# Performance work log

Hardware: AMD Instinct MI355X
Metric: run time of the kernel (lower is better)

The kernel has to match this reference:

```python
import jax, jax.numpy as jnp
import numpy as np

MEM_DIM = 2048
MEM_FEAT = 512
N_TOKENS = 65536
ALPHA = 0.1
SOFTMAX_SCALE = 10.0


def _l2_normalize(x, axis, eps=1e-12):
    # matches tf.math.l2_normalize: x / sqrt(max(sum(x^2), eps))
    sq = jnp.sum(jnp.square(x), axis=axis, keepdims=True)
    return x * jax.lax.rsqrt(jnp.maximum(sq, eps))


def setup_inputs() -> dict:
    key = jax.random.key(0)
    k1, k2 = jax.random.split(key)
    inputs = jax.random.normal(k1, (N_TOKENS, MEM_FEAT), dtype=jnp.float32)
    memory = jax.random.normal(k2, (MEM_DIM, MEM_FEAT), dtype=jnp.float32) * 0.05
    return {"inputs": inputs, "memory": memory}


def reference(inputs, memory):
    inputs_norm = _l2_normalize(inputs, axis=1)            # [N, F]
    memory_norm = _l2_normalize(memory, axis=1)            # [M, F]
    cos_sim = jnp.einsum('nf,mf->nm', inputs_norm, memory_norm)  # [N, M]
    attn = jax.nn.softmax(cos_sim * SOFTMAX_SCALE, axis=1)       # [N, M]
    mem_update = jnp.einsum('nm,mf->nf', attn, memory_norm)      # [N, F]
    closest_idx = jnp.argmax(attn, axis=1)                       # [N]
    # one_hot^T @ inputs_norm == segment-sum of inputs_norm by closest code
    memory_updates = jax.ops.segment_sum(inputs_norm, closest_idx,
                                         num_segments=MEM_DIM)  # [M, F]
    updated_memory = memory * (1.0 - ALPHA) + memory_updates * ALPHA
    return mem_update, updated_memory
```

## Files before the change

### kernel.cpp

```cpp
#include <hip/hip_runtime.h>
#include <stdint.h>

#define N_TOK   65536
#define MDIM    2048
#define FDIM    512
#define SCALE_F 10.0f
#define TAU_BF  1.2e-3f
#define TAU_SP  2e-5f
#define QCAP    8192

typedef __attribute__((ext_vector_type(8))) unsigned short u16x8;
typedef __attribute__((ext_vector_type(4))) unsigned short u16x4;
typedef __attribute__((ext_vector_type(8))) __bf16 bf16x8;
typedef __attribute__((ext_vector_type(4))) float f32x4;

__device__ __forceinline__ unsigned short f2bf(float f) {
  unsigned int u = __builtin_bit_cast(unsigned int, f);
  u += 0x7fffu + ((u >> 16) & 1u);
  return (unsigned short)(u >> 16);
}
__device__ __forceinline__ float bf2f(unsigned short b) {
  return __builtin_bit_cast(float, (unsigned int)b << 16);
}
__device__ __forceinline__ f32x4 mfma16(u16x8 a, u16x8 b, f32x4 c) {
  return __builtin_amdgcn_mfma_f32_16x16x32_bf16(
      __builtin_bit_cast(bf16x8, a), __builtin_bit_cast(bf16x8, b), c, 0, 0, 0);
}
__device__ __forceinline__ void gload16(const unsigned short* g, unsigned short* l) {
  __builtin_amdgcn_global_load_lds(
      (const __attribute__((address_space(1))) unsigned int*)g,
      (__attribute__((address_space(3))) unsigned int*)l,
      16, 0, 0);
}
__device__ __forceinline__ unsigned long long packkey(float x, int col) {
  unsigned u = __builtin_bit_cast(unsigned, x);
  u = (u & 0x80000000u) ? ~u : (u | 0x80000000u);
  return ((unsigned long long)u << 32) | (unsigned)(2048 - col);
}
__device__ __forceinline__ float unpackval(unsigned long long k) {
  unsigned u = (unsigned)(k >> 32);
  u = (u & 0x80000000u) ? (u & 0x7fffffffu) : ~u;
  return __builtin_bit_cast(float, u);
}
__device__ __forceinline__ int unpackcol(unsigned long long k) {
  return 2048 - (int)(k & 0xffffffffu);
}
__device__ __forceinline__ void merge2(unsigned long long& k1, unsigned long long& k2,
                                       unsigned long long o1, unsigned long long o2) {
  if (o1 > k1) { k2 = (k1 > o2) ? k1 : o2; k1 = o1; }
  else if (o1 > k2) { k2 = o1; }
}

__global__ __launch_bounds__(64) void zero_k(int* __restrict__ qcount) {
  if (threadIdx.x == 0) *qcount = 0;
}

__global__ __launch_bounds__(64) void prep_memory_k(
    const float* __restrict__ mem, unsigned short* __restrict__ Bh,
    unsigned short* __restrict__ Bl) {
  const int m = blockIdx.x;
  const int lane = threadIdx.x;
  const float* row = mem + (size_t)m * FDIM;
  float4 a = *(const float4*)(row + lane * 4);
  float4 b = *(const float4*)(row + 256 + lane * 4);
  float s = a.x * a.x + a.y * a.y + a.z * a.z + a.w * a.w +
            b.x * b.x + b.y * b.y + b.z * b.z + b.w * b.w;
  #pragma unroll
  for (int off = 1; off < 64; off <<= 1) s += __shfl_xor(s, off);
  const float rn = 1.0f / sqrtf(fmaxf(s, 1e-12f));
  float v[8] = {a.x, a.y, a.z, a.w, b.x, b.y, b.z, b.w};
  #pragma unroll
  for (int h = 0; h < 2; ++h) {
    ushort4 hs, lo;
    #pragma unroll
    for (int q = 0; q < 4; ++q) {
      float x = v[h * 4 + q] * rn;
      unsigned short hb = f2bf(x);
      ((unsigned short*)&hs)[q] = hb;
      ((unsigned short*)&lo)[q] = f2bf(x - bf2f(hb));
    }
    const size_t e = (size_t)m * FDIM + h * 256 + lane * 4;
    *(ushort4*)(Bh + e) = hs;
    *(ushort4*)(Bl + e) = lo;
  }
}

__global__ __launch_bounds__(256) void transpose_k(
    const unsigned short* __restrict__ Bh, unsigned short* __restrict__ Bt) {
  __shared__ unsigned short t[32][33];
  const int m0 = blockIdx.x * 32, f0 = blockIdx.y * 32;
  const int tx = threadIdx.x & 31, ty = threadIdx.x >> 5;
  #pragma unroll
  for (int r = ty; r < 32; r += 8)
    t[r][tx] = Bh[(size_t)(m0 + r) * FDIM + f0 + tx];
  __syncthreads();
  #pragma unroll
  for (int r = ty; r < 32; r += 8)
    Bt[(size_t)(f0 + r) * MDIM + m0 + tx] = t[tx][r];
}

__global__ __launch_bounds__(256) void prep_a_k(
    const float* __restrict__ inp, float* __restrict__ inv_n,
    unsigned short* __restrict__ Ah, int baseRow) {
  const int r = blockIdx.x * 4 + (threadIdx.x >> 6);
  const int lane = threadIdx.x & 63;
  const int grow = baseRow + r;
  const float* x = inp + (size_t)grow * FDIM;
  float4 a = *(const float4*)(x + lane * 4);
  float4 b = *(const float4*)(x + 256 + lane * 4);
  float s = a.x * a.x + a.y * a.y + a.z * a.z + a.w * a.w +
            b.x * b.x + b.y * b.y + b.z * b.z + b.w * b.w;
  #pragma unroll
  for (int off = 1; off < 64; off <<= 1) s += __shfl_xor(s, off);
  const float rn = 1.0f / sqrtf(fmaxf(s, 1e-12f));
  if (lane == 0) inv_n[grow] = rn;
  ushort4 h0, h1;
  h0.x = f2bf(a.x * rn); h0.y = f2bf(a.y * rn);
  h0.z = f2bf(a.z * rn); h0.w = f2bf(a.w * rn);
  h1.x = f2bf(b.x * rn); h1.y = f2bf(b.y * rn);
  h1.z = f2bf(b.z * rn); h1.w = f2bf(b.w * rn);
  *(ushort4*)(Ah + (size_t)r * FDIM + lane * 4) = h0;
  *(ushort4*)(Ah + (size_t)r * FDIM + 256 + lane * 4) = h1;
}

template <int MODE>
__global__ __launch_bounds__(512) void gemm8p_k(
    const unsigned short* __restrict__ Am, const unsigned short* __restrict__ Bm,
    void* __restrict__ Cv, int N, int K, int nbxLog2,
    float* __restrict__ ssum, unsigned long long* __restrict__ sk1,
    unsigned long long* __restrict__ sk2, const float* __restrict__ rowinv) {
  __shared__ alignas(16) char smem[131072];
  int wg = blockIdx.x;
  { const int q = gridDim.x >> 3; wg = (wg & 7) * q + (wg >> 3); }
  const int bx = wg & ((1 << nbxLog2) - 1);
  const int by = wg >> nbxLog2;
  const int m0 = by * 256, n0 = bx * 256;
  const int tid = threadIdx.x;
  const int lane = tid & 63, wid = tid >> 6;
  const int wm = wid >> 2, wn = wid & 3;
  const int lr = lane & 15, ls = lane >> 4;
  const int c16 = (lane & 7) ^ (lane >> 3);
  const int lrow8 = lane >> 3;

  f32x4 acc[8][4] = {};
  u16x8 bF[4][2];

  const int NT = K >> 6;
  const int niter = NT >> 1;

  auto stageB = [&](int t, int half) {
    char* dst0 = smem + (t & 1) * 65536 + 32768 + half * 16384;
    #pragma unroll
    for (int c = 0; c < 2; ++c) {
      const int R = (wid * 2 + c) * 8;
      const int rg = n0 + half * 128 + R + lrow8;
      gload16(Bm + (size_t)rg * K + t * 64 + c16 * 8,
              (unsigned short*)(dst0 + R * 128));
    }
  };
  auto stageA = [&](int t, int q) {
    const int half = wid >> 2;
    const int R = q * 32 + (wid & 3) * 8;
    char* dst = smem + (t & 1) * 65536 + half * 16384 + R * 128;
    const int rg = m0 + half * 128 + R + lrow8;
    gload16(Am + (size_t)rg * K + t * 64 + c16 * 8, (unsigned short*)dst);
  };
  auto ldsA = [&](int b, int rl, int ks) -> u16x8 {
    const int p = (ks * 4 + ls) ^ (rl & 7);
    return *(const u16x8*)(smem + b * 65536 + wm * 16384 + rl * 128 + p * 16);
  };
  auto ldsB = [&](int b, int rlb, int ks) -> u16x8 {
    const int half = rlb >> 7, rl = rlb & 127;
    const int p = (ks * 4 + ls) ^ (rl & 7);
    return *(const u16x8*)(smem + b * 65536 + 32768 + half * 16384 + rl * 128 + p * 16);
  };

  stageB(0, 0); stageB(0, 1);
  stageA(0, 0); stageA(0, 1); stageA(0, 2); stageA(0, 3);
  stageB(1, 0); stageB(1, 1);
  stageA(1, 0); stageA(1, 1); stageA(1, 2);

  for (int it = 0; it < niter; ++it) {
    const int T0 = 2 * it, T1 = T0 + 1;
    #pragma unroll
    for (int ph = 0; ph < 8; ++ph) {
      const int tb = (ph < 4) ? 0 : 1;
      const int ql = ph & 3;
      if (ql == 0) {
        if (ph == 4 && it == niter - 1)
          asm volatile("s_waitcnt vmcnt(0)" ::: "memory");
        else
          asm volatile("s_waitcnt vmcnt(7)" ::: "memory");
        __builtin_amdgcn_sched_barrier(0);
        __builtin_amdgcn_s_barrier();
        #pragma unroll
        for (int nj = 0; nj < 4; ++nj)
          #pragma unroll
          for (int ks = 0; ks < 2; ++ks)
            bF[nj][ks] = ldsB(tb, wn * 64 + nj * 16 + lr, ks);
      } else {
        __builtin_amdgcn_s_barrier();
      }
      u16x8 aF[2][2];
      #pragma unroll
      for (int di = 0; di < 2; ++di)
        #pragma unroll
        for (int ks = 0; ks < 2; ++ks)
          aF[di][ks] = ldsA(tb, ql * 32 + di * 16 + lr, ks);
      if (ph == 0) { if (T1 < NT) stageA(T1, 3); }
      if (ph == 1) { if (T0 + 2 < NT) stageB(T0 + 2, 0); }
      if (ph == 2) { if (T0 + 2 < NT) { stageB(T0 + 2, 1); stageA(T0 + 2, 0); } }
      if (ph == 3) { if (T0 + 2 < NT) { stageA(T0 + 2, 1); stageA(T0 + 2, 2); } }
      if (ph == 4) { if (T0 + 2 < NT) stageA(T0 + 2, 3); }
      if (ph == 5) { if (T1 + 2 < NT) stageB(T1 + 2, 0); }
      if (ph == 6) { if (T1 + 2 < NT) { stageB(T1 + 2, 1); stageA(T1 + 2, 0); } }
      if (ph == 7) { if (T1 + 2 < NT) { stageA(T1 + 2, 1); stageA(T1 + 2, 2); } }
      __builtin_amdgcn_s_setprio(1);
      #pragma unroll
      for (int di = 0; di < 2; ++di)
        #pragma unroll
        for (int nj = 0; nj < 4; ++nj)
          #pragma unroll
          for (int ks = 0; ks < 2; ++ks)
            acc[ql * 2 + di][nj] = mfma16(aF[di][ks], bF[nj][ks], acc[ql * 2 + di][nj]);
      __builtin_amdgcn_s_setprio(0);
      __builtin_amdgcn_s_barrier();
    }
  }

  if constexpr (MODE == 1) {
    asm volatile("s_waitcnt vmcnt(0)" ::: "memory");
    __builtin_amdgcn_sched_barrier(0);
    __builtin_amdgcn_s_barrier();
    unsigned short* P = (unsigned short*)Cv;
    float* sc = (float*)smem;
    #pragma unroll
    for (int g = 0; g < 8; ++g) {
      if ((wid >> 2) == (g >> 2)) {
        const int di0 = (g & 3) * 2;
        #pragma unroll
        for (int di = 0; di < 2; ++di)
          #pragma unroll
          for (int nj = 0; nj < 4; ++nj)
            #pragma unroll
            for (int q = 0; q < 4; ++q)
              sc[(di * 16 + ls * 4 + q) * 260 + wn * 64 + nj * 16 + lr] =
                  acc[di0 + di][nj][q];
      }
      __syncthreads();
      {
        const int r = tid >> 4, cs = tid & 15;
        const int grow = m0 + g * 32 + r;
        float esum = 0.f, m1v = -3.4e38f, m2v = -3.4e38f;
        int c1 = 0;
        unsigned short pk[16];
        #pragma unroll
        for (int k = 0; k < 4; ++k) {
          const f32x4 v = *(const f32x4*)&sc[r * 260 + cs * 16 + k * 4];
          #pragma unroll
          for (int e = 0; e < 4; ++e) {
            const float s = v[e];
            const int col = n0 + cs * 16 + k * 4 + e;
            if (s > m1v) { m2v = m1v; m1v = s; c1 = col; }
            else if (s > m2v) m2v = s;
            const float ex = __expf(SCALE_F * s);
            esum += ex;
            pk[k * 4 + e] = f2bf(ex);
          }
        }
        *(u16x8*)&P[(size_t)grow * N + n0 + cs * 16] = *(u16x8*)&pk[0];
        *(u16x8*)&P[(size_t)grow * N + n0 + cs * 16 + 8] = *(u16x8*)&pk[8];
        unsigned long long k1 = packkey(m1v, c1);
        unsigned long long k2 = packkey(m2v, 2047);
        #pragma unroll
        for (int off = 1; off < 16; off <<= 1) {
          const unsigned long long o1 = __shfl_xor(k1, off);
          const unsigned long long o2 = __shfl_xor(k2, off);
          esum += __shfl_xor(esum, off);
          merge2(k1, k2, o1, o2);
        }
        if (cs == 0) {
          const size_t sp = (size_t)grow * 8 + bx;
          ssum[sp] = esum; sk1[sp] = k1; sk2[sp] = k2;
        }
      }
      __syncthreads();
    }
  } else {
    float* C = (float*)Cv;
    #pragma unroll
    for (int mi = 0; mi < 8; ++mi) {
      const int rbase = m0 + wm * 128 + mi * 16 + ls * 4;
      #pragma unroll
      for (int q = 0; q < 4; ++q) {
        const float ri = rowinv[rbase + q];
        #pragma unroll
        for (int nj = 0; nj < 4; ++nj) {
          const int col = n0 + wn * 64 + nj * 16 + lr;
          C[(size_t)(rbase + q) * N + col] = acc[mi][nj][q] * ri;
        }
      }
    }
  }
}

__global__ __launch_bounds__(256) void gemm_ref_k(
    const unsigned short* __restrict__ Ah, const unsigned short* __restrict__ Al,
    const unsigned short* __restrict__ Bh, const unsigned short* __restrict__ Bl,
    float* __restrict__ C, int N, int K, int nbxLog2,
    const int* __restrict__ qlimit) {
  const int wg = blockIdx.x;
  const int bx = wg & ((1 << nbxLog2) - 1);
  const int by = wg >> nbxLog2;
  const int m0 = by * 128, n0 = bx * 128;
  {
    int lim = *qlimit; if (lim > QCAP) lim = QCAP;
    lim = (lim + 127) & ~127;
    if (m0 >= lim) return;
  }
  constexpr int BUF_B = 4 * 8192;
  __shared__ alignas(16) char smem[2 * BUF_B];

  const int tid = threadIdx.x;
  const int lane = tid & 63, wave = tid >> 6;
  const int wr = wave >> 1, wc = wave & 1;
  const int lr = lane & 15, ls = lane >> 4;

  f32x4 acc[4][4] = {};

  const int row0 = wave * 32 + (lane >> 2);
  const int row1 = row0 + 16;
  const int ce = (lane & 3) * 8;
  const unsigned short* gA0 = Ah + (size_t)(m0 + row0) * K + ce;
  const unsigned short* gA1 = Ah + (size_t)(m0 + row1) * K + ce;
  const unsigned short* gB0 = Bh + (size_t)(n0 + row0) * K + ce;
  const unsigned short* gB1 = Bh + (size_t)(n0 + row1) * K + ce;
  const unsigned short* gAl0 = Al + (size_t)(m0 + row0) * K + ce;
  const unsigned short* gAl1 = Al + (size_t)(m0 + row1) * K + ce;
  const unsigned short* gBl0 = Bl + (size_t)(n0 + row0) * K + ce;
  const unsigned short* gBl1 = Bl + (size_t)(n0 + row1) * K + ce;

  auto stage = [&](int buf) {
    char* sb = smem + buf * BUF_B;
    unsigned short* bAh = (unsigned short*)sb;
    unsigned short* bBh = (unsigned short*)(sb + 8192);
    unsigned short* bAl = (unsigned short*)(sb + 16384);
    unsigned short* bBl = (unsigned short*)(sb + 24576);
    gload16(gA0, &bAh[wave * 1024]); gload16(gA1, &bAh[wave * 1024 + 512]);
    gload16(gB0, &bBh[wave * 1024]); gload16(gB1, &bBh[wave * 1024 + 512]);
    gload16(gAl0, &bAl[wave * 1024]); gload16(gAl1, &bAl[wave * 1024 + 512]);
    gload16(gBl0, &bBl[wave * 1024]); gload16(gBl1, &bBl[wave * 1024 + 512]);
    gA0 += 32; gA1 += 32; gB0 += 32; gB1 += 32;
    gAl0 += 32; gAl1 += 32; gBl0 += 32; gBl1 += 32;
  };

  const int nk = K >> 5;
  stage(0);
  __syncthreads();
  for (int ks = 0; ks < nk; ++ks) {
    const int cur = ks & 1;
    if (ks + 1 < nk) stage(cur ^ 1);
    const char* sb = smem + cur * BUF_B;
    u16x8 fa[4], fb[4], fal[4], fbl[4];
    #pragma unroll
    for (int i = 0; i < 4; ++i) {
      const int ra = (wr * 64 + i * 16 + lr) * 32 + ls * 8;
      const int rb = (wc * 64 + i * 16 + lr) * 32 + ls * 8;
      fa[i] = *(const u16x8*)&((const unsigned short*)sb)[ra];
      fb[i] = *(const u16x8*)&((const unsigned short*)(sb + 8192))[rb];
      fal[i] = *(const u16x8*)&((const unsigned short*)(sb + 16384))[ra];
      fbl[i] = *(const u16x8*)&((const unsigned short*)(sb + 24576))[rb];
    }
    #pragma unroll
    for (int i = 0; i < 4; ++i)
      #pragma unroll
      for (int j = 0; j < 4; ++j) {
        acc[i][j] = mfma16(fa[i], fb[j], acc[i][j]);
        acc[i][j] = mfma16(fal[i], fb[j], acc[i][j]);
        acc[i][j] = mfma16(fa[i], fbl[j], acc[i][j]);
      }
    __syncthreads();
  }

  #pragma unroll
  for (int i = 0; i < 4; ++i) {
    const int rrow = m0 + wr * 64 + i * 16 + ls * 4;
    #pragma unroll
    for (int j = 0; j < 4; ++j) {
      const int col = n0 + wc * 64 + j * 16 + lr;
      #pragma unroll
      for (int q = 0; q < 4; ++q)
        C[(size_t)(rrow + q) * N + col] = acc[i][j][q];
    }
  }
}

__global__ __launch_bounds__(256) void rowstat_k(
    const float* __restrict__ ssum, const unsigned long long* __restrict__ sk1,
    const unsigned long long* __restrict__ sk2, int* __restrict__ idx,
    float* __restrict__ rowinv, int* __restrict__ queue,
    int* __restrict__ qcount, int baseRow) {
  const int row = blockIdx.x * 32 + (threadIdx.x >> 3);
  const int p = threadIdx.x & 7;
  const size_t sp = (size_t)row * 8 + p;
  float sum = ssum[sp];
  unsigned long long k1 = sk1[sp], k2 = sk2[sp];
  #pragma unroll
  for (int off = 1; off < 8; off <<= 1) {
    const unsigned long long o1 = __shfl_xor(k1, off);
    const unsigned long long o2 = __shfl_xor(k2, off);
    sum += __shfl_xor(sum, off);
    merge2(k1, k2, o1, o2);
  }
  if (p == 0) {
    const int tok = baseRow + row;
    idx[tok] = unpackcol(k1);
    rowinv[row] = 1.0f / sum;
    if (unpackval(k1) - unpackval(k2) < TAU_BF) {
      int slot = atomicAdd(qcount, 1);
      if (slot < QCAP) queue[slot] = tok;
    }
  }
}

__global__ __launch_bounds__(256) void gather_prep_k(
    const int* __restrict__ queue, const int* __restrict__ qcount,
    const float* __restrict__ inp, const float* __restrict__ inv_n,
    unsigned short* __restrict__ Qh, unsigned short* __restrict__ Ql) {
  const int w = blockIdx.x * 4 + (threadIdx.x >> 6);
  const int lane = threadIdx.x & 63;
  int cnt = *qcount; if (cnt > QCAP) cnt = QCAP;
  if (w >= cnt) return;
  const int tok = queue[w];
  const float rn = inv_n[tok];
  const float* x = inp + (size_t)tok * FDIM;
  #pragma unroll
  for (int h = 0; h < 2; ++h) {
    float4 xv = *(const float4*)(x + h * 256 + lane * 4);
    float vv[4] = {xv.x, xv.y, xv.z, xv.w};
    ushort4 hs, lo;
    #pragma unroll
    for (int q = 0; q < 4; ++q) {
      float v = vv[q] * rn;
      unsigned short hb = f2bf(v);
      ((unsigned short*)&hs)[q] = hb;
      ((unsigned short*)&lo)[q] = f2bf(v - bf2f(hb));
    }
    const size_t e = (size_t)w * FDIM + h * 256 + lane * 4;
    *(ushort4*)(Qh + e) = hs;
    *(ushort4*)(Ql + e) = lo;
  }
}

__global__ __launch_bounds__(256) void refine2_k(
    const int* __restrict__ queue, const int* __restrict__ qcount,
    const float* __restrict__ Sref, const float* __restrict__ inp,
    const float* __restrict__ mem, int* __restrict__ idx) {
  const int w = blockIdx.x * 4 + (threadIdx.x >> 6);
  const int lane = threadIdx.x & 63;
  int cnt = *qcount; if (cnt > QCAP) cnt = QCAP;
  if (w >= cnt) return;
  const int tok = queue[w];
  const float* srow = Sref + (size_t)w * MDIM;
  float m1 = -3.4e38f, m2 = -3.4e38f;
  int i1 = 0x7fffffff, i2 = 0x7fffffff;
  #pragma unroll
  for (int i = 0; i < 8; ++i) {
    const float4 vv = *(const float4*)(srow + i * 256 + lane * 4);
    const float xs[4] = {vv.x, vv.y, vv.z, vv.w};
    #pragma unroll
    for (int q = 0; q < 4; ++q) {
      const float x = xs[q];
      const int ii = i * 256 + lane * 4 + q;
      if (x > m1 || (x == m1 && ii < i1)) { m2 = m1; i2 = i1; m1 = x; i1 = ii; }
      else if (x > m2 || (x == m2 && ii < i2)) { m2 = x; i2 = ii; }
    }
  }
  #pragma unroll
  for (int off = 1; off < 64; off <<= 1) {
    const float n1 = __shfl_xor(m1, off), n2 = __shfl_xor(m2, off);
    const int j1 = __shfl_xor(i1, off), j2 = __shfl_xor(i2, off);
    if (n1 > m1 || (n1 == m1 && j1 < i1)) {
      if (m1 > n2 || (m1 == n2 && i1 < j2)) { m2 = m1; i2 = i1; }
      else { m2 = n2; i2 = j2; }
      m1 = n1; i1 = j1;
    } else if (n1 > m2 || (n1 == m2 && j1 < i2)) { m2 = n1; i2 = j1; }
  }
  int pick = i1;
  if (m1 - m2 < TAU_SP) {
    const int a = (i1 < i2) ? i1 : i2, b = (i1 < i2) ? i2 : i1;
    const float* x = inp + (size_t)tok * FDIM;
    const float* ma = mem + (size_t)a * FDIM;
    const float* mb = mem + (size_t)b * FDIM;
    double da = 0, db = 0, na = 0, nb = 0;
    #pragma unroll
    for (int j = 0; j < 8; ++j) {
      const int e = lane * 8 + j;
      const double xv = x[e], av = ma[e], bv = mb[e];
      da += xv * av; na += av * av;
      db += xv * bv; nb += bv * bv;
    }
    #pragma unroll
    for (int off = 1; off < 64; off <<= 1) {
      da += __shfl_xor(da, off); na += __shfl_xor(na, off);
      db += __shfl_xor(db, off); nb += __shfl_xor(nb, off);
    }
    const double d1 = da / sqrt(fmax(na, 1e-12));
    const double d2 = db / sqrt(fmax(nb, 1e-12));
    if (d2 > d1) pick = b;
    else pick = a;
  }
  if (lane == 0) idx[tok] = pick;
}

__global__ __launch_bounds__(256) void segsum_k(
    const int* __restrict__ idx, const float* __restrict__ inp,
    const float* __restrict__ inv_n, float* __restrict__ updates) {
  __shared__ int lst[256];
  __shared__ int lcnt;
  const int m = blockIdx.x;
  const int t = threadIdx.x;
  float a0 = 0.f, a1 = 0.f;
  for (int base = 0; base < N_TOK; base += 4096) {
    if (t == 0) lcnt = 0;
    __syncthreads();
    #pragma unroll
    for (int u = 0; u < 4; ++u) {
      const int off4 = (u * 256 + t) * 4;
      const int4 v = *(const int4*)&idx[base + off4];
      if (v.x == m) { int p = atomicAdd(&lcnt, 1); if (p < 256) lst[p] = base + off4 + 0; }
      if (v.y == m) { int p = atomicAdd(&lcnt, 1); if (p < 256) lst[p] = base + off4 + 1; }
      if (v.z == m) { int p = atomicAdd(&lcnt, 1); if (p < 256) lst[p] = base + off4 + 2; }
      if (v.w == m) { int p = atomicAdd(&lcnt, 1); if (p < 256) lst[p] = base + off4 + 3; }
    }
    __syncthreads();
    int c = lcnt; if (c > 256) c = 256;
    if (t == 0 && c > 1) {
      for (int i = 1; i < c; ++i) {
        int key = lst[i], j = i - 1;
        while (j >= 0 && lst[j] > key) { lst[j + 1] = lst[j]; --j; }
        lst[j + 1] = key;
      }
    }
    __syncthreads();
    for (int i = 0; i < c; ++i) {
      const int tok = lst[i];
      const float rn = inv_n[tok];
      const float2 xv = *(const float2*)&inp[(size_t)tok * FDIM + t * 2];
      a0 += xv.x * rn; a1 += xv.y * rn;
    }
    __syncthreads();
  }
  *(float2*)&updates[(size_t)m * FDIM + t * 2] = make_float2(a0, a1);
}

__global__ __launch_bounds__(256) void final_update_k(
    const float* __restrict__ mem, const float* __restrict__ upd,
    float* __restrict__ out) {
  const size_t i = ((size_t)blockIdx.x * 256 + threadIdx.x) * 4;
  float4 m = *(const float4*)(mem + i);
  float4 u = *(const float4*)(upd + i);
  float4 r;
  r.x = m.x * 0.9f + u.x * 0.1f;
  r.y = m.y * 0.9f + u.y * 0.1f;
  r.z = m.z * 0.9f + u.z * 0.1f;
  r.w = m.w * 0.9f + u.w * 0.1f;
  *(float4*)(out + i) = r;
}

extern "C" void kernel_launch(void* const* d_in, const int* in_sizes, int n_in,
                              void* d_out, int out_size, void* d_ws, size_t ws_size,
                              hipStream_t stream) {
  const float* inputs = (const float*)d_in[0];
  const float* memory = (const float*)d_in[1];
  if (n_in >= 2 && in_sizes[0] != N_TOK * FDIM) {
    inputs = (const float*)d_in[1];
    memory = (const float*)d_in[0];
  }
  float* out_mu = (float*)d_out;
  float* out_um = out_mu + (size_t)N_TOK * FDIM;

  char* base = (char*)d_ws;
  size_t off = 0;
  auto take = [&](size_t bytes) -> char* {
    char* p = base + off;
    off = (off + bytes + 255) & ~(size_t)255;
    return p;
  };
  unsigned short* Bh = (unsigned short*)take((size_t)MDIM * FDIM * 2);
  unsigned short* Bl = (unsigned short*)take((size_t)MDIM * FDIM * 2);
  unsigned short* Bt = (unsigned short*)take((size_t)MDIM * FDIM * 2);
  float* inv_n = (float*)take((size_t)N_TOK * 4);
  float* updates = (float*)take((size_t)MDIM * FDIM * 4);
  int* idx = (int*)take((size_t)N_TOK * 4);
  int* queue = (int*)take((size_t)QCAP * 4);
  int* qcount = (int*)take(256);
  unsigned short* Qh = (unsigned short*)take((size_t)QCAP * FDIM * 2);
  unsigned short* Ql = (unsigned short*)take((size_t)QCAP * FDIM * 2);
  float* Sref = (float*)take((size_t)QCAP * MDIM * 4);
  const size_t fixed = off;

  int chunkT = 65536;
  while (chunkT > 2048 && fixed + (size_t)chunkT * 5400 + 8192 > ws_size)
    chunkT >>= 1;
  if (fixed + (size_t)chunkT * 5400 + 8192 > ws_size) return;

  unsigned short* Ah = (unsigned short*)take((size_t)chunkT * FDIM * 2);
  unsigned short* Pbuf = (unsigned short*)take((size_t)chunkT * MDIM * 2);
  float* ssum = (float*)take((size_t)chunkT * 8 * 4);
  unsigned long long* sk1 = (unsigned long long*)take((size_t)chunkT * 8 * 8);
  unsigned long long* sk2 = (unsigned long long*)take((size_t)chunkT * 8 * 8);
  float* rowinv = (float*)take((size_t)chunkT * 4);

  zero_k<<<1, 64, 0, stream>>>(qcount);
  prep_memory_k<<<MDIM, 64, 0, stream>>>(memory, Bh, Bl);
  transpose_k<<<dim3(MDIM / 32, FDIM / 32), 256, 0, stream>>>(Bh, Bt);

  for (int baseRow = 0; baseRow < N_TOK; baseRow += chunkT) {
    prep_a_k<<<chunkT / 4, 256, 0, stream>>>(inputs, inv_n, Ah, baseRow);
    gemm8p_k<1><<<(chunkT / 256) * 8, 512, 0, stream>>>(
        Ah, Bh, (void*)Pbuf, MDIM, FDIM, 3, ssum, sk1, sk2, nullptr);
    rowstat_k<<<chunkT / 32, 256, 0, stream>>>(
        ssum, sk1, sk2, idx, rowinv, queue, qcount, baseRow);
    gemm8p_k<2><<<(chunkT / 256) * 2, 512, 0, stream>>>(
        Pbuf, Bt, (void*)(out_mu + (size_t)baseRow * FDIM), FDIM, MDIM, 1,
        nullptr, nullptr, nullptr, rowinv);
  }
  gather_prep_k<<<QCAP / 4, 256, 0, stream>>>(queue, qcount, inputs, inv_n, Qh, Ql);
  gemm_ref_k<<<16 * (QCAP / 128), 256, 0, stream>>>(
      Qh, Ql, Bh, Bl, Sref, MDIM, FDIM, 4, qcount);
  refine2_k<<<QCAP / 4, 256, 0, stream>>>(queue, qcount, Sref, inputs, memory, idx);
  segsum_k<<<MDIM, 256, 0, stream>>>(idx, inputs, inv_n, updates);
  final_update_k<<<(MDIM * FDIM / 4) / 256, 256, 0, stream>>>(memory, updates, out_um);
}
```

Before: 718.7 us.

## Loop each GEMM1 workgroup over all column tiles with continuous prefetch pipeline

The first GEMM now launches one persistent workgroup per 256-row block that walks all eight 256-column segments of memory in one continuous K-pipeline. Each segment's softmax/argmax epilogue runs in place through a separate 16 KB swizzled LDS scratch, while the next segment's tiles are already being prefetched. This removes per-tile prologue/epilogue pipeline drains and the A-tile reloads across workgroups. The cost is an 8x smaller grid (256 workgroups at full size), more LDS per block, and an epilogue that now sits inside the main loop.

```diff
diff --git a/kernel.cpp b/kernel.cpp
--- a/kernel.cpp
+++ b/kernel.cpp
@@ -123,18 +123,22 @@
   *(ushort4*)(Ah + (size_t)r * FDIM + 256 + lane * 4) = h1;
 }
 
-template <int MODE>
+template <int MODE, int SEGS, int NTL>
 __global__ __launch_bounds__(512) void gemm8p_k(
     const unsigned short* __restrict__ Am, const unsigned short* __restrict__ Bm,
     void* __restrict__ Cv, int N, int K, int nbxLog2,
     float* __restrict__ ssum, unsigned long long* __restrict__ sk1,
     unsigned long long* __restrict__ sk2, const float* __restrict__ rowinv) {
-  __shared__ alignas(16) char smem[131072];
+  constexpr int NTSEG = 1 << NTL;
+  constexpr int NTT = SEGS * NTSEG;
+  constexpr int NITER = NTT / 2;
+  __shared__ alignas(16) char smem[(MODE == 1) ? 147456 : 131072];
   int wg = blockIdx.x;
   { const int q = gridDim.x >> 3; wg = (wg & 7) * q + (wg >> 3); }
-  const int bx = wg & ((1 << nbxLog2) - 1);
-  const int by = wg >> nbxLog2;
-  const int m0 = by * 256, n0 = bx * 256;
+  int by, bx0 = 0;
+  if constexpr (SEGS > 1) { by = wg; }
+  else { bx0 = wg & ((1 << nbxLog2) - 1); by = wg >> nbxLog2; }
+  const int m0 = by * 256;
   const int tid = threadIdx.x;
   const int lane = tid & 63, wid = tid >> 6;
   const int wm = wid >> 2, wn = wid & 3;
@@ -145,25 +149,25 @@
   f32x4 acc[8][4] = {};
   u16x8 bF[4][2];
 
-  const int NT = K >> 6;
-  const int niter = NT >> 1;
-
-  auto stageB = [&](int t, int half) {
-    char* dst0 = smem + (t & 1) * 65536 + 32768 + half * 16384;
+  auto stageB = [&](int T, int half) {
+    const int n0 = (SEGS > 1 ? (T >> NTL) : bx0) * 256;
+    const int ko = (T & (NTSEG - 1)) * 64;
+    char* dst0 = smem + (T & 1) * 65536 + 32768 + half * 16384;
     #pragma unroll
     for (int c = 0; c < 2; ++c) {
       const int R = (wid * 2 + c) * 8;
       const int rg = n0 + half * 128 + R + lrow8;
-      gload16(Bm + (size_t)rg * K + t * 64 + c16 * 8,
+      gload16(Bm + (size_t)rg * K + ko + c16 * 8,
               (unsigned short*)(dst0 + R * 128));
     }
   };
-  auto stageA = [&](int t, int q) {
+  auto stageA = [&](int T, int q) {
+    const int ko = (T & (NTSEG - 1)) * 64;
     const int half = wid >> 2;
     const int R = q * 32 + (wid & 3) * 8;
-    char* dst = smem + (t & 1) * 65536 + half * 16384 + R * 128;
+    char* dst = smem + (T & 1) * 65536 + half * 16384 + R * 128;
     const int rg = m0 + half * 128 + R + lrow8;
-    gload16(Am + (size_t)rg * K + t * 64 + c16 * 8, (unsigned short*)dst);
+    gload16(Am + (size_t)rg * K + ko + c16 * 8, (unsigned short*)dst);
   };
   auto ldsA = [&](int b, int rl, int ks) -> u16x8 {
     const int p = (ks * 4 + ls) ^ (rl & 7);
@@ -180,14 +184,14 @@
   stageB(1, 0); stageB(1, 1);
   stageA(1, 0); stageA(1, 1); stageA(1, 2);
 
-  for (int it = 0; it < niter; ++it) {
+  for (int it = 0; it < NITER; ++it) {
     const int T0 = 2 * it, T1 = T0 + 1;
     #pragma unroll
     for (int ph = 0; ph < 8; ++ph) {
       const int tb = (ph < 4) ? 0 : 1;
       const int ql = ph & 3;
       if (ql == 0) {
-        if (ph == 4 && it == niter - 1)
+        if (ph == 4 && it == NITER - 1)
           asm volatile("s_waitcnt vmcnt(0)" ::: "memory");
         else
           asm volatile("s_waitcnt vmcnt(7)" ::: "memory");
@@ -207,14 +211,14 @@
         #pragma unroll
         for (int ks = 0; ks < 2; ++ks)
           aF[di][ks] = ldsA(tb, ql * 32 + di * 16 + lr, ks);
-      if (ph == 0) { if (T1 < NT) stageA(T1, 3); }
-      if (ph == 1) { if (T0 + 2 < NT) stageB(T0 + 2, 0); }
-      if (ph == 2) { if (T0 + 2 < NT) { stageB(T0 + 2, 1); stageA(T0 + 2, 0); } }
-      if (ph == 3) { if (T0 + 2 < NT) { stageA(T0 + 2, 1); stageA(T0 + 2, 2); } }
-      if (ph == 4) { if (T0 + 2 < NT) stageA(T0 + 2, 3); }
-      if (ph == 5) { if (T1 + 2 < NT) stageB(T1 + 2, 0); }
-      if (ph == 6) { if (T1 + 2 < NT) { stageB(T1 + 2, 1); stageA(T1 + 2, 0); } }
-      if (ph == 7) { if (T1 + 2 < NT) { stageA(T1 + 2, 1); stageA(T1 + 2, 2); } }
+      if (ph == 0) { if (T1 < NTT) stageA(T1, 3); }
+      if (ph == 1) { if (T0 + 2 < NTT) stageB(T0 + 2, 0); }
+      if (ph == 2) { if (T0 + 2 < NTT) { stageB(T0 + 2, 1); stageA(T0 + 2, 0); } }
+      if (ph == 3) { if (T0 + 2 < NTT) { stageA(T0 + 2, 1); stageA(T0 + 2, 2); } }
+      if (ph == 4) { if (T0 + 2 < NTT) stageA(T0 + 2, 3); }
+      if (ph == 5) { if (T1 + 2 < NTT) stageB(T1 + 2, 0); }
+      if (ph == 6) { if (T1 + 2 < NTT) { stageB(T1 + 2, 1); stageA(T1 + 2, 0); } }
+      if (ph == 7) { if (T1 + 2 < NTT) { stageA(T1 + 2, 1); stageA(T1 + 2, 2); } }
       __builtin_amdgcn_s_setprio(1);
       #pragma unroll
       for (int di = 0; di < 2; ++di)
@@ -226,68 +230,76 @@
       __builtin_amdgcn_s_setprio(0);
       __builtin_amdgcn_s_barrier();
     }
-  }
-
-  if constexpr (MODE == 1) {
-    asm volatile("s_waitcnt vmcnt(0)" ::: "memory");
-    __builtin_amdgcn_sched_barrier(0);
-    __builtin_amdgcn_s_barrier();
-    unsigned short* P = (unsigned short*)Cv;
-    float* sc = (float*)smem;
-    #pragma unroll
-    for (int g = 0; g < 8; ++g) {
-      if ((wid >> 2) == (g >> 2)) {
-        const int di0 = (g & 3) * 2;
+    if constexpr (MODE == 1) {
+      if (((it + 1) & ((NTSEG >> 1) - 1)) == 0) {
+        const int seg = it >> (NTL - 1);
+        const int n0e = seg * 256;
+        float* sc = (float*)(smem + 131072);
+        unsigned short* P = (unsigned short*)Cv;
         #pragma unroll
-        for (int di = 0; di < 2; ++di)
+        for (int g = 0; g < 16; ++g) {
+          __syncthreads();
+          if (wm == (g >> 3)) {
+            const int mi = g & 7;
+            #pragma unroll
+            for (int nj = 0; nj < 4; ++nj)
+              #pragma unroll
+              for (int q = 0; q < 4; ++q) {
+                const int row = ls * 4 + q;
+                const int col = wn * 64 + nj * 16 + lr;
+                sc[row * 256 + (((col >> 2) ^ (row & 7)) * 4) + (col & 3)] =
+                    acc[mi][nj][q];
+              }
+          }
+          __syncthreads();
+          const int r = tid >> 5, cs = tid & 31;
+          const int grow = m0 + g * 16 + r;
+          float esum = 0.f, m1v = -3.4e38f, m2v = -3.4e38f;
+          int c1 = 0;
+          unsigned short pk[8];
+          #pragma unroll
+          for (int k = 0; k < 2; ++k) {
+            const int slot = k * 32 + cs;
+            const f32x4 v = *(const f32x4*)&sc[r * 256 + ((slot ^ (r & 7)) * 4)];
+            #pragma unroll
+            for (int e = 0; e < 4; ++e) {
+              const float s = v[e];
+              const int col = n0e + slot * 4 + e;
+              if (s > m1v) { m2v = m1v; m1v = s; c1 = col; }
+              else if (s > m2v) m2v = s;
+              const float ex = __expf(SCALE_F * s);
+              esum += ex;
+              pk[k * 4 + e] = f2bf(ex);
+            }
+          }
+          *(u16x4*)&P[(size_t)grow * N + n0e + cs * 4] = *(u16x4*)&pk[0];
+          *(u16x4*)&P[(size_t)grow * N + n0e + 128 + cs * 4] = *(u16x4*)&pk[4];
+          unsigned long long k1 = packkey(m1v, c1);
+          unsigned long long k2 = packkey(m2v, 2047);
+          #pragma unroll
+          for (int off = 1; off < 32; off <<= 1) {
+            const unsigned long long o1 = __shfl_xor(k1, off);
+            const unsigned long long o2 = __shfl_xor(k2, off);
+            esum += __shfl_xor(esum, off);
+            merge2(k1, k2, o1, o2);
+          }
+          if (cs == 0) {
+            const size_t sp = (size_t)grow * 8 + seg;
+            ssum[sp] = esum; sk1[sp] = k1; sk2[sp] = k2;
+          }
+        }
+        #pragma unroll
+        for (int mi = 0; mi < 8; ++mi)
           #pragma unroll
           for (int nj = 0; nj < 4; ++nj)
-            #pragma unroll
-            for (int q = 0; q < 4; ++q)
-              sc[(di * 16 + ls * 4 + q) * 260 + wn * 64 + nj * 16 + lr] =
-                  acc[di0 + di][nj][q];
+            acc[mi][nj] = (f32x4){0.f, 0.f, 0.f, 0.f};
       }
-      __syncthreads();
-      {
-        const int r = tid >> 4, cs = tid & 15;
-        const int grow = m0 + g * 32 + r;
-        float esum = 0.f, m1v = -3.4e38f, m2v = -3.4e38f;
-        int c1 = 0;
-        unsigned short pk[16];
-        #pragma unroll
-        for (int k = 0; k < 4; ++k) {
-          const f32x4 v = *(const f32x4*)&sc[r * 260 + cs * 16 + k * 4];
-          #pragma unroll
-          for (int e = 0; e < 4; ++e) {
-            const float s = v[e];
-            const int col = n0 + cs * 16 + k * 4 + e;
-            if (s > m1v) { m2v = m1v; m1v = s; c1 = col; }
-            else if (s > m2v) m2v = s;
-            const float ex = __expf(SCALE_F * s);
-            esum += ex;
-            pk[k * 4 + e] = f2bf(ex);
-          }
-        }
-        *(u16x8*)&P[(size_t)grow * N + n0 + cs * 16] = *(u16x8*)&pk[0];
-        *(u16x8*)&P[(size_t)grow * N + n0 + cs * 16 + 8] = *(u16x8*)&pk[8];
-        unsigned long long k1 = packkey(m1v, c1);
-        unsigned long long k2 = packkey(m2v, 2047);
-        #pragma unroll
-        for (int off = 1; off < 16; off <<= 1) {
-          const unsigned long long o1 = __shfl_xor(k1, off);
-          const unsigned long long o2 = __shfl_xor(k2, off);
-          esum += __shfl_xor(esum, off);
-          merge2(k1, k2, o1, o2);
-        }
-        if (cs == 0) {
-          const size_t sp = (size_t)grow * 8 + bx;
-          ssum[sp] = esum; sk1[sp] = k1; sk2[sp] = k2;
-        }
-      }
-      __syncthreads();
-    }
-  } else {
+    }
+  }
+
+  if constexpr (MODE == 2) {
     float* C = (float*)Cv;
+    const int n0 = bx0 * 256;
     #pragma unroll
     for (int mi = 0; mi < 8; ++mi) {
       const int rbase = m0 + wm * 128 + mi * 16 + ls * 4;
@@ -618,11 +630,11 @@
 
   for (int baseRow = 0; baseRow < N_TOK; baseRow += chunkT) {
     prep_a_k<<<chunkT / 4, 256, 0, stream>>>(inputs, inv_n, Ah, baseRow);
-    gemm8p_k<1><<<(chunkT / 256) * 8, 512, 0, stream>>>(
-        Ah, Bh, (void*)Pbuf, MDIM, FDIM, 3, ssum, sk1, sk2, nullptr);
+    gemm8p_k<1, 8, 3><<<chunkT / 256, 512, 0, stream>>>(
+        Ah, Bh, (void*)Pbuf, MDIM, FDIM, 0, ssum, sk1, sk2, nullptr);
     rowstat_k<<<chunkT / 32, 256, 0, stream>>>(
         ssum, sk1, sk2, idx, rowinv, queue, qcount, baseRow);
-    gemm8p_k<2><<<(chunkT / 256) * 2, 512, 0, stream>>>(
+    gemm8p_k<2, 1, 5><<<(chunkT / 256) * 2, 512, 0, stream>>>(
         Pbuf, Bt, (void*)(out_mu + (size_t)baseRow * FDIM), FDIM, MDIM, 1,
         nullptr, nullptr, nullptr, rowinv);
   }
```

Result: slower. 994.8 us (+38.4%).
